# Optimization experiments

Measured on AMD Instinct MI355X. Metric: run time of the kernel, lower is better.

Reference implementation:

```python
import jax, jax.numpy as jnp
import numpy as np
from jax import lax

PRE_NMS = 2000
POST_NMS = 300
NMS_THRESH = 0.7
MIN_SIZE = 16.0
SCALE = 1.0
RATIOS = (0.5, 1.0, 2.0)
SCALES = (8, 16, 32)
STRIDES = (8, 16, 32)
FEAT_HW = ((100, 100), (50, 50), (25, 25))
BASE_SIZE = 16.0


def _anchor_base(scale):
    py = px = BASE_SIZE / 2.0
    ab = np.zeros((len(RATIOS), 4), dtype=np.float32)
    for i, r in enumerate(RATIOS):
        h = BASE_SIZE * scale * np.sqrt(r)
        w = BASE_SIZE * scale * np.sqrt(1.0 / r)
        ab[i] = [py - h / 2.0, px - w / 2.0, py + h / 2.0, px + w / 2.0]
    return ab


def _enum_anchors():
    out = []
    for lvl in range(3):
        ab = _anchor_base(SCALES[lvl])
        hh, ww = FEAT_HW[lvl]
        fs = STRIDES[lvl]
        sy = np.arange(0, hh * fs, fs)
        sx = np.arange(0, ww * fs, fs)
        sx, sy = np.meshgrid(sx, sy)
        shift = np.stack((sy.ravel(), sx.ravel(), sy.ravel(), sx.ravel()), axis=1)
        a = ab[None, :, :] + shift[:, None, :]  # [K, A, 4]
        out.append(a.reshape(-1, 4).astype(np.float32))
    return np.concatenate(out, axis=0)  # [39375, 4]


def setup_inputs() -> dict:
    key = jax.random.key(0)
    ks = jax.random.split(key, 8)
    inp = {
        "feat0": jax.random.normal(ks[0], (2, 256, 100, 100), jnp.float32),
        "feat1": jax.random.normal(ks[1], (2, 256, 50, 50), jnp.float32),
        "feat2": jax.random.normal(ks[2], (2, 256, 25, 25), jnp.float32),
        "conv_w": 0.01 * jax.random.normal(ks[3], (256, 256, 3, 3), jnp.float32),
        "conv_b": jnp.zeros((256,), jnp.float32),
        "score_w": 0.01 * jax.random.normal(ks[4], (6, 256), jnp.float32),
        "score_b": jnp.zeros((6,), jnp.float32),
        "loc_w": 0.01 * jax.random.normal(ks[5], (12, 256), jnp.float32),
        "loc_b": jnp.zeros((12,), jnp.float32),
        "anchors": jnp.asarray(_enum_anchors()),
        "img_h": 800,
        "img_w": 800,
    }
    return inp


def loc2bbox(anchors, loc):
    src_h = anchors[:, 2] - anchors[:, 0]
    src_w = anchors[:, 3] - anchors[:, 1]
    ctr_y = anchors[:, 0] + 0.5 * src_h
    ctr_x = anchors[:, 1] + 0.5 * src_w
    dy, dx, dh, dw = loc[:, 0], loc[:, 1], loc[:, 2], loc[:, 3]
    cy = dy * src_h + ctr_y
    cx = dx * src_w + ctr_x
    h = jnp.exp(dh) * src_h
    w = jnp.exp(dw) * src_w
    return jnp.stack([cy - 0.5 * h, cx - 0.5 * w, cy + 0.5 * h, cx + 0.5 * w], axis=1)


def _iou_matrix(boxes):
    area = (boxes[:, 2] - boxes[:, 0]) * (boxes[:, 3] - boxes[:, 1])
    tl = jnp.maximum(boxes[:, None, :2], boxes[None, :, :2])
    br = jnp.minimum(boxes[:, None, 2:], boxes[None, :, 2:])
    wh = jnp.clip(br - tl, 0.0)
    inter = wh[..., 0] * wh[..., 1]
    return inter / (area[:, None] + area[None, :] - inter + 1e-12)


def _nms_keep(boxes, valid):
    # greedy NMS over score-sorted boxes; returns boolean keep mask
    M = _iou_matrix(boxes)  # [PRE_NMS, PRE_NMS]
    idx = jnp.arange(PRE_NMS)

    def body(i, suppressed):
        sup_later = (~suppressed[i]) & (M[i] > NMS_THRESH) & (idx > i)
        return suppressed | sup_later

    suppressed = lax.fori_loop(0, PRE_NMS, body, ~valid)
    return ~suppressed


def _propose(loc, fg, anchors, img_h, img_w):
    roi = loc2bbox(anchors, loc)  # [S, 4]
    roi = jnp.stack([
        jnp.clip(roi[:, 0], 0.0, float(img_h)),
        jnp.clip(roi[:, 1], 0.0, float(img_w)),
        jnp.clip(roi[:, 2], 0.0, float(img_h)),
        jnp.clip(roi[:, 3], 0.0, float(img_w)),
    ], axis=1)
    hs = roi[:, 2] - roi[:, 0]
    ws = roi[:, 3] - roi[:, 1]
    valid = (hs >= MIN_SIZE * SCALE) & (ws >= MIN_SIZE * SCALE)
    sc = jnp.where(valid, fg, -jnp.inf)
    top_sc, top_idx = lax.top_k(sc, PRE_NMS)
    boxes = roi[top_idx]
    keep = _nms_keep(boxes, jnp.isfinite(top_sc))
    # stable move of kept boxes to the front (indices are unique)
    order = jnp.argsort(jnp.where(keep, jnp.arange(PRE_NMS), PRE_NMS))[:POST_NMS]
    rois = boxes[order] * keep[order][:, None].astype(boxes.dtype)  # zero-pad invalid
    return rois  # [POST_NMS, 4]


def reference(feat0, feat1, feat2, conv_w, conv_b, score_w, score_b, loc_w, loc_b, anchors, img_h, img_w):
    feats = [feat0, feat1, feat2]
    n = feat0.shape[0]
    locs, scores, fgs = [], [], []
    dn = ("NCHW", "OIHW", "NCHW")
    for x in feats:
        h = jax.nn.relu(
            lax.conv_general_dilated(x, conv_w, (1, 1), "SAME", dimension_numbers=dn)
            + conv_b[None, :, None, None]
        )
        hh, ww = h.shape[2], h.shape[3]
        loc = jnp.einsum("nchw,oc->nhwo", h, loc_w) + loc_b  # [n,h,w,12]
        sc = jnp.einsum("nchw,oc->nhwo", h, score_w) + score_b  # [n,h,w,6]
        fg = jax.nn.softmax(sc.reshape(n, hh, ww, 3, 2), axis=-1)[..., 1]
        locs.append(loc.reshape(n, -1, 4))
        scores.append(sc.reshape(n, -1, 2))
        fgs.append(fg.reshape(n, -1))
    rpn_locs = jnp.concatenate(locs, axis=1)      # [n, S, 4]
    rpn_scores = jnp.concatenate(scores, axis=1)  # [n, S, 2]
    rpn_fg = jnp.concatenate(fgs, axis=1)         # [n, S]
    rois = jax.vmap(lambda l, f: _propose(l, f, anchors, img_h, img_w))(rpn_locs, rpn_fg)
    rois = rois.reshape(-1, 4)  # [n*POST_NMS, 4]
    roi_indices = jnp.repeat(jnp.arange(n, dtype=jnp.int32), POST_NMS)
    return rpn_locs, rpn_scores, rois, roi_indices, anchors
```

## Files before the change

kernel.cpp:

```cpp
#include <hip/hip_runtime.h>
#include <hip/hip_fp16.h>
#include <cstdint>
#include <cstddef>

typedef unsigned long long u64;
typedef unsigned int u32;
typedef __attribute__((ext_vector_type(8))) _Float16 f16x8;
typedef __attribute__((ext_vector_type(4))) float f32x4;

#define NANCHORS 39375
#define PRE_NMS  2000
#define POST_NMS 300
#define CAND_CAP 4096
#define MPAD 2048
#define UNEG 0x007FFFFFu
#define NPIX 26250

__device__ __forceinline__ u32 f2u(float f) {
  u32 u = __float_as_uint(f);
  return (u & 0x80000000u) ? ~u : (u | 0x80000000u);
}

#define GLOAD16(gp, lp) __builtin_amdgcn_global_load_lds( \
    (const __attribute__((address_space(1))) u32*)(const void*)(gp), \
    (__attribute__((address_space(3))) u32*)(void*)(lp), 16, 0, 0)

#define DPP_SUM16(v) do { \
  v += __int_as_float(__builtin_amdgcn_update_dpp(0, __float_as_int(v), 0x128, 0xf, 0xf, true)); \
  v += __int_as_float(__builtin_amdgcn_update_dpp(0, __float_as_int(v), 0x124, 0xf, 0xf, true)); \
  v += __int_as_float(__builtin_amdgcn_update_dpp(0, __float_as_int(v), 0x122, 0xf, 0xf, true)); \
  v += __int_as_float(__builtin_amdgcn_update_dpp(0, __float_as_int(v), 0x121, 0xf, 0xf, true)); \
} while (0)

__global__ __launch_bounds__(64) void ringzero_kernel(short* __restrict__ xh, short* __restrict__ xl) {
  int t = blockIdx.x;
  int b = t / 712, i = t % 712;
  int W2, AB, ABS;
  if (i < 404)      { W2 = 102; AB = 0;       ABS = 2663424; }
  else if (i < 608) { i -= 404; W2 = 52; AB = 5326848; ABS = 692224; }
  else              { i -= 608; W2 = 27; AB = 6711296; ABS = 186624; }
  int y, x;
  if (i < W2)          { y = 0;      x = i; }
  else if (i < 2 * W2) { y = W2 - 1; x = i - W2; }
  else { int j = i - 2 * W2; y = 1 + (j >> 1); x = (j & 1) ? (W2 - 1) : 0; }
  size_t base = (size_t)AB + (size_t)b * ABS + ((size_t)(y * W2 + x)) * 256 + threadIdx.x * 4;
  int2 z = {0, 0};
  *(int2*)(xh + base) = z;
  *(int2*)(xl + base) = z;
}

__global__ __launch_bounds__(256) void xsplit_kernel(
    const float* __restrict__ f0, const float* __restrict__ f1, const float* __restrict__ f2,
    short* __restrict__ xh, short* __restrict__ xl)
{
  __shared__ float tile[64][65];
  int t = blockIdx.x;
  int HW, W, W2, np; const float* fp; int AB, ABS;
  if (t < 1256)      { HW = 10000; W = 100; W2 = 102; np = 157; fp = f0; AB = 0;       ABS = 2663424; }
  else if (t < 1576) { t -= 1256; HW = 2500; W = 50; W2 = 52; np = 40; fp = f1; AB = 5326848; ABS = 692224; }
  else               { t -= 1576; HW = 625;  W = 25; W2 = 27; np = 10; fp = f2; AB = 6711296; ABS = 186624; }
  int posb = t % np, r = t / np;
  int ci0 = (r & 3) * 64, b = r >> 2;
  int pos0 = posb * 64;
  int tid = threadIdx.x, lane = tid & 63, w = tid >> 6;
  int rp = pos0 + lane; if (rp >= HW) rp = HW - 1;
  const float* src = fp + (size_t)(b * 256 + ci0) * HW;
#pragma unroll
  for (int p = 0; p < 16; ++p) {
    int cl = w * 16 + p;
    tile[cl][lane] = src[(size_t)cl * HW + rp];
  }
  __syncthreads();
  int pix = tid >> 2, cq = tid & 3;
  int pos = pos0 + pix;
  if (pos < HW) {
    int y = pos / W, x = pos - y * W;
    size_t ob = (size_t)AB + (size_t)b * ABS + ((size_t)((y + 1) * W2 + (x + 1))) * 256 + ci0 + cq * 16;
    __align__(16) short hs[16], ls[16];
#pragma unroll
    for (int j = 0; j < 16; ++j) {
      float v = tile[cq * 16 + j][pix];
      __half h = __float2half(v);
      __half l = __float2half((v - __half2float(h)) * 2048.0f);
      hs[j] = __half_as_short(h);
      ls[j] = __half_as_short(l);
    }
    *(int4*)(xh + ob) = ((int4*)hs)[0];
    *(int4*)(xh + ob + 8) = ((int4*)hs)[1];
    *(int4*)(xl + ob) = ((int4*)ls)[0];
    *(int4*)(xl + ob + 8) = ((int4*)ls)[1];
  }
}

__global__ __launch_bounds__(256) void wsplit_kernel(
    const float* __restrict__ w, short* __restrict__ wh, short* __restrict__ wl)
{
  int idx = blockIdx.x * 256 + threadIdx.x;
  int tap = idx >> 16, co = (idx >> 8) & 255, ci = idx & 255;
  float v = w[(size_t)co * 2304 + ci * 9 + tap];
  __half h = __float2half(v);
  __half l = __float2half((v - __half2float(h)) * 2048.0f);
  wh[idx] = __half_as_short(h);
  wl[idx] = __half_as_short(l);
}

__global__ __launch_bounds__(256, 2) void gemmconv_kernel(
    const short* __restrict__ xh, const short* __restrict__ xl,
    const short* __restrict__ wh, const short* __restrict__ wl,
    const float* __restrict__ bias,
    const float* __restrict__ loc_w, const float* __restrict__ score_w,
    float* __restrict__ proj2)
{
  __shared__ __align__(16) short smem[32768];

  int lb = (blockIdx.x & 7) * 52 + (blockIdx.x >> 3);
  int HW, W, W2, AB, ABS, lvlbase;
  if (lb < 316)      { HW = 10000; W = 100; W2 = 102; AB = 0;       ABS = 2663424; lvlbase = 0; }
  else if (lb < 396) { lb -= 316; HW = 2500; W = 50; W2 = 52; AB = 5326848; ABS = 692224; lvlbase = 10000; }
  else               { lb -= 396; HW = 625;  W = 25; W2 = 27; AB = 6711296; ABS = 186624; lvlbase = 12500; }
  int mb = lb >> 2, b = (lb >> 1) & 1, nb = lb & 1;
  int pos0 = mb * 128, co0 = nb * 128;

  int tid = threadIdx.x;
  int s = tid & 7, mrow = tid >> 3;
  int aoff[4], boff[4];
#pragma unroll
  for (int i = 0; i < 4; ++i) {
    int m = i * 32 + mrow;
    int pos = pos0 + m; if (pos >= HW) pos = HW - 1;
    int y = pos / W, x = pos - y * W;
    aoff[i] = AB + b * ABS + (y * W2 + x) * 256 + ((s ^ (m & 7)) << 3);
    boff[i] = ((co0 + m) << 8) + ((s ^ (m & 7)) << 3);
  }
  int wv = tid >> 6, lane = tid & 63;
  int lr = lane & 15, lk = lane >> 4;
  int wr = wv >> 1, wc = wv & 1;
  int rA0 = wr * 64 + lr, rB0 = wc * 64 + lr;
  int cs = (lr & 7) << 4;
  int c0 = ((lk * 16) ^ cs) >> 1;
  int c1 = ((64 + lk * 16) ^ cs) >> 1;

  f32x4 acc1[4][4], acc2[4][4];
  f32x4 zro = {0.f, 0.f, 0.f, 0.f};
#pragma unroll
  for (int i = 0; i < 4; ++i)
#pragma unroll
    for (int j = 0; j < 4; ++j) { acc1[i][j] = zro; acc2[i][j] = zro; }

  for (int cc = 0; cc < 36; ++cc) {
    int tap = cc >> 2, cq = cc & 3;
    int ty = tap / 3, tx = tap - ty * 3;
    int adel = (ty * W2 + tx) * 256 + (cq << 6);
    int bdel = (tap << 16) + (cq << 6);
    if (cc) __syncthreads();
#pragma unroll
    for (int i = 0; i < 4; ++i) {
      int d = i * 2048 + wv * 512;
      GLOAD16(xh + aoff[i] + adel, smem + d);
      GLOAD16(xl + aoff[i] + adel, smem + 8192 + d);
      GLOAD16(wh + boff[i] + bdel, smem + 16384 + d);
      GLOAD16(wl + boff[i] + bdel, smem + 24576 + d);
    }
    __syncthreads();
#pragma unroll
    for (int k2 = 0; k2 < 2; ++k2) {
      int ck = k2 ? c1 : c0;
      f16x8 ah[4], al[4], bh[4], bl[4];
#pragma unroll
      for (int q = 0; q < 4; ++q) {
        int ro = (rA0 + q * 16) * 64 + ck;
        ah[q] = *(const f16x8*)(smem + ro);
        al[q] = *(const f16x8*)(smem + 8192 + ro);
        int rb = (rB0 + q * 16) * 64 + ck;
        bh[q] = *(const f16x8*)(smem + 16384 + rb);
        bl[q] = *(const f16x8*)(smem + 24576 + rb);
      }
#pragma unroll
      for (int m4 = 0; m4 < 4; ++m4)
#pragma unroll
        for (int n4 = 0; n4 < 4; ++n4) {
          acc1[m4][n4] = __builtin_amdgcn_mfma_f32_16x16x32_f16(ah[m4], bh[n4], acc1[m4][n4], 0, 0, 0);
          acc2[m4][n4] = __builtin_amdgcn_mfma_f32_16x16x32_f16(ah[m4], bl[n4], acc2[m4][n4], 0, 0, 0);
          acc2[m4][n4] = __builtin_amdgcn_mfma_f32_16x16x32_f16(al[m4], bh[n4], acc2[m4][n4], 0, 0, 0);
        }
    }
  }

  float br[4];
#pragma unroll
  for (int n4 = 0; n4 < 4; ++n4) br[n4] = bias[co0 + wc * 64 + n4 * 16 + lr];
  float* pslot = proj2 + (size_t)(nb * 2 + wc) * NPIX * 20;
  int Pbase = b * 13125 + lvlbase;

#pragma unroll 1
  for (int half = 0; half < 2; ++half) {
    float wpr[4][9];
#pragma unroll
    for (int n4 = 0; n4 < 4; ++n4) {
      int c = co0 + wc * 64 + n4 * 16 + lr;
#pragma unroll
      for (int oo = 0; oo < 9; ++oo) {
        int o = half * 9 + oo;
        wpr[n4][oo] = (o < 12) ? loc_w[o * 256 + c] : score_w[(o - 12) * 256 + c];
      }
    }
#pragma unroll
    for (int m4 = 0; m4 < 4; ++m4) {
#pragma unroll
      for (int j = 0; j < 4; ++j) {
        int pos = pos0 + wr * 64 + m4 * 16 + lk * 4 + j;
        bool ok = pos < HW;
        float po[9];
#pragma unroll
        for (int oo = 0; oo < 9; ++oo) po[oo] = 0.f;
#pragma unroll
        for (int n4 = 0; n4 < 4; ++n4) {
          float h = acc1[m4][n4][j] + acc2[m4][n4][j] * 4.8828125e-4f + br[n4];
          h = ok ? fmaxf(h, 0.f) : 0.f;
#pragma unroll
          for (int oo = 0; oo < 9; ++oo) po[oo] = fmaf(h, wpr[n4][oo], po[oo]);
        }
#pragma unroll
        for (int oo = 0; oo < 9; ++oo) DPP_SUM16(po[oo]);
        if (ok && lr < 9) {
          float out = po[0];
#pragma unroll
          for (int oo = 1; oo < 9; ++oo) if (lr == oo) out = po[oo];
          pslot[(size_t)(Pbase + pos) * 20 + half * 9 + lr] = out;
        }
      }
    }
  }
}

__global__ __launch_bounds__(256) void decode_kernel(
    const float* __restrict__ proj2, const float* __restrict__ loc_b, const float* __restrict__ score_b,
    const float* __restrict__ anchors, const int* __restrict__ imgh, const int* __restrict__ imgw,
    float* __restrict__ out_locs, float* __restrict__ out_scores,
    float* __restrict__ boxes, u32* __restrict__ ukey)
{
  int P = blockIdx.x * 256 + threadIdx.x;
  if (P >= NPIX) return;
  int b = P / 13125, r = P % 13125;
  int pos, base_row;
  if (r < 10000)      { pos = r;         base_row = 0; }
  else if (r < 12500) { pos = r - 10000; base_row = 30000; }
  else                { pos = r - 12500; base_row = 37500; }

  float sarr[18];
#pragma unroll
  for (int o = 0; o < 18; ++o)
    sarr[o] = proj2[(size_t)P * 20 + o] + proj2[(size_t)NPIX * 20 + (size_t)P * 20 + o]
            + proj2[(size_t)2 * NPIX * 20 + (size_t)P * 20 + o]
            + proj2[(size_t)3 * NPIX * 20 + (size_t)P * 20 + o];

  float IH = (float)(*imgh), IW = (float)(*imgw);
#pragma unroll
  for (int a = 0; a < 3; ++a) {
    float l0 = sarr[4 * a + 0] + loc_b[4 * a + 0];
    float l1 = sarr[4 * a + 1] + loc_b[4 * a + 1];
    float l2 = sarr[4 * a + 2] + loc_b[4 * a + 2];
    float l3 = sarr[4 * a + 3] + loc_b[4 * a + 3];
    float sc0 = sarr[12 + 2 * a + 0] + score_b[2 * a + 0];
    float sc1 = sarr[12 + 2 * a + 1] + score_b[2 * a + 1];

    int row = base_row + pos * 3 + a;
    size_t g = (size_t)b * NANCHORS + row;
    *(float4*)(out_locs + g * 4) = make_float4(l0, l1, l2, l3);
    out_scores[g * 2 + 0] = sc0; out_scores[g * 2 + 1] = sc1;

    float mx = fmaxf(sc0, sc1);
    float e0 = expf(sc0 - mx), e1 = expf(sc1 - mx);
    float fg = e1 / (e0 + e1);

    const float* an = anchors + (size_t)row * 4;
    float a0 = an[0], a1 = an[1], a2 = an[2], a3 = an[3];
    float sh = a2 - a0, sw = a3 - a1;
    float cy = a0 + 0.5f * sh, cx = a1 + 0.5f * sw;
    float ncy = l0 * sh + cy, ncx = l1 * sw + cx;
    float nh = expf(l2) * sh, nw = expf(l3) * sw;
    float y1 = fminf(fmaxf(ncy - 0.5f * nh, 0.f), IH);
    float x1 = fminf(fmaxf(ncx - 0.5f * nw, 0.f), IW);
    float y2 = fminf(fmaxf(ncy + 0.5f * nh, 0.f), IH);
    float x2 = fminf(fmaxf(ncx + 0.5f * nw, 0.f), IW);
    bool valid = ((y2 - y1) >= 16.0f) && ((x2 - x1) >= 16.0f);
    float scm = valid ? fg : -__builtin_inff();

    *(float4*)(boxes + g * 4) = make_float4(y1, x1, y2, x2);
    ukey[g] = f2u(scm);
  }
}

__global__ void copyf_kernel(const float* __restrict__ a, float* __restrict__ o, int n) {
  int t = blockIdx.x * 256 + threadIdx.x;
  if (t < n) o[t] = a[t];
}

__global__ __launch_bounds__(1024) void selectsort_kernel(
    const u32* __restrict__ ukey, const float* __restrict__ boxes,
    float* __restrict__ topbox, u64* __restrict__ sup0)
{
  int b = blockIdx.x, tid = threadIdx.x;
  int lane = tid & 63;
  const u32* u = ukey + (size_t)b * NANCHORS;
  __shared__ u32 hist[256];
  __shared__ u32 sh_prefix;
  __shared__ int sh_rem;
  __shared__ int sh_cnt;
  __shared__ u64 key[CAND_CAP];
  __shared__ unsigned char validf[2048];

  u32 val[39];
#pragma unroll
  for (int k = 0; k < 38; ++k) val[k] = u[tid + k * 1024];
  val[38] = (tid < 463) ? u[tid + 38912] : 0u;

  u32 prefix = 0; int rem = PRE_NMS;
#pragma unroll 1
  for (int pass = 0; pass < 4; ++pass) {
    int shift = 24 - 8 * pass;
    if (tid < 256) hist[tid] = 0;
    __syncthreads();
    u32 himask = (pass == 0) ? 0u : (0xFFFFFFFFu << (shift + 8));
    u32 pmask = prefix & himask;
#pragma unroll
    for (int k = 0; k < 39; ++k) {
      bool live = (k < 38) || (tid < 463);
      u32 v = val[k];
      bool m = live && ((v & himask) == pmask);
      u32 bin = (v >> shift) & 255u;
      u64 actm = __ballot(m);
      if (actm) {
        int src = __ffsll(actm) - 1;
        u32 binf = __shfl(bin, src, 64);
        bool same = m && (bin == binf);
        u64 sm = __ballot(same);
        if (same) {
          if (lane == __ffsll(sm) - 1)
            atomicAdd(&hist[binf], (u32)__popcll(sm));
        } else if (m) {
          atomicAdd(&hist[bin], 1u);
        }
      }
    }
    __syncthreads();
    if (tid < 64) {
      u32 h0 = hist[4 * lane], h1 = hist[4 * lane + 1];
      u32 h2 = hist[4 * lane + 2], h3 = hist[4 * lane + 3];
      u32 L = h0 + h1 + h2 + h3;
      u32 SS = L;
#pragma unroll
      for (int off = 1; off < 64; off <<= 1) {
        u32 tv = __shfl_down(SS, off, 64);
        if (lane + off < 64) SS += tv;
      }
      u32 T = SS - L;
      u32 s3 = h3 + T, s2 = h2 + s3, s1 = h1 + s2, s0 = h0 + s1;
      u32 sv[5] = {s0, s1, s2, s3, T};
#pragma unroll
      for (int j = 0; j < 4; ++j) {
        if ((int)sv[j] >= rem && (int)sv[j + 1] < rem) {
          sh_prefix = prefix | ((u32)(4 * lane + j) << shift);
          sh_rem = rem - (int)sv[j + 1];
        }
      }
    }
    __syncthreads();
    prefix = sh_prefix; rem = sh_rem;
  }

  if (tid == 0) sh_cnt = 0;
  __syncthreads();
#pragma unroll
  for (int k = 0; k < 39; ++k) {
    bool live = (k < 38) || (tid < 463);
    u32 v = val[k];
    bool c = live && (v >= prefix);
    u64 mask = __ballot(c);
    if (mask) {
      int leader = __ffsll(mask) - 1;
      int cntw = __popcll(mask);
      int base = 0;
      if (lane == leader) base = atomicAdd(&sh_cnt, cntw);
      base = __shfl(base, leader, 64);
      int p = base + (int)__popcll(mask & ((1ull << lane) - 1ull));
      if (c && p < CAND_CAP)
        key[p] = ((u64)v << 32) | (u32)(~(u32)(tid + k * 1024));
    }
  }
  __syncthreads();
  int cnt = (sh_cnt < CAND_CAP) ? sh_cnt : CAND_CAP;
  for (int t = tid; t < CAND_CAP; t += 1024)
    if (t >= cnt) key[t] = 0ull;
  __syncthreads();

  u32 n = (cnt <= 2048) ? 2048u : (u32)CAND_CAP;
  for (u32 k = 2; k <= n; k <<= 1) {
    for (u32 j = k >> 1; j > 0; j >>= 1) {
      __syncthreads();
      for (u32 t = tid; t < n; t += 1024) {
        u32 ixj = t ^ j;
        if (ixj > t) {
          u64 a = key[t], c = key[ixj];
          bool desc = ((t & k) == 0);
          if (desc ? (a < c) : (a > c)) { key[t] = c; key[ixj] = a; }
        }
      }
    }
  }
  __syncthreads();

  for (int t = tid; t < 2048; t += 1024) {
    unsigned char vf = 0;
    if (t < PRE_NMS) {
      u64 kk = key[t];
      u32 uu = (u32)(kk >> 32);
      float* tb = topbox + ((size_t)b * PRE_NMS + t) * 4;
      if (uu != 0u) {
        u32 idx = ~((u32)kk);
        const float* bp = boxes + ((size_t)b * NANCHORS + idx) * 4;
        tb[0] = bp[0]; tb[1] = bp[1]; tb[2] = bp[2]; tb[3] = bp[3];
        vf = (uu != UNEG) ? 1 : 0;
      } else {
        tb[0] = 0.f; tb[1] = 0.f; tb[2] = 0.f; tb[3] = 0.f;
      }
    }
    validf[t] = vf;
  }
  __syncthreads();
  if (tid < 32) {
    u64 m = 0;
    for (int bit = 0; bit < 64; ++bit) {
      int j = tid * 64 + bit;
      if (j >= PRE_NMS || !validf[j]) m |= (1ull << bit);
    }
    sup0[b * 32 + tid] = m;
  }
}

__global__ __launch_bounds__(256) void iou_kernel(const float* __restrict__ topbox, u32* __restrict__ M32)
{
  int t = blockIdx.x * 256 + threadIdx.x;
  int b = blockIdx.y;
  int w = t / 2000, i = t % 2000;
  const float* tb = topbox + (size_t)b * PRE_NMS * 4;
  const float* bi = tb + (size_t)i * 4;
  float iy1 = bi[0], ix1 = bi[1], iy2 = bi[2], ix2 = bi[3];
  float ai = (iy2 - iy1) * (ix2 - ix1);
  u64 m = 0;
  for (int bit = 0; bit < 64; ++bit) {
    int j = w * 64 + bit;
    if (j < PRE_NMS && j > i) {
      const float* bj = tb + (size_t)j * 4;
      float ty = fmaxf(iy1, bj[0]), tx = fmaxf(ix1, bj[1]);
      float by = fminf(iy2, bj[2]), bx = fminf(ix2, bj[3]);
      float hh = fmaxf(by - ty, 0.f), ww = fmaxf(bx - tx, 0.f);
      float inter = hh * ww;
      float aj = (bj[2] - bj[0]) * (bj[3] - bj[1]);
      float iou = inter / (ai + aj - inter + 1e-12f);
      if (iou > 0.7f) m |= (1ull << bit);
    }
  }
  u32* out = M32 + (size_t)b * MPAD * 64;
  out[(size_t)(2 * w)     * MPAD + i] = (u32)m;
  out[(size_t)(2 * w + 1) * MPAD + i] = (u32)(m >> 32);
}

__global__ __launch_bounds__(320) void final_kernel(
    const u32* __restrict__ M32, const u64* __restrict__ sup0, const float* __restrict__ topbox,
    float* __restrict__ rois, float* __restrict__ roiidx)
{
  int b = blockIdx.x, tid = threadIdx.x;
  __shared__ u32 supl[64];
  __shared__ int ord[POST_NMS];
  __shared__ int cnt_s;

  if (tid < 64) {
    int l = tid;
    const u32* col = M32 + (size_t)b * MPAD * 64 + (size_t)l * MPAD;
    u32 sup = ((const u32*)sup0)[b * 64 + l];
    uint4 A[16], B[16];
#pragma unroll
    for (int k = 0; k < 16; ++k) A[k] = *(const uint4*)(col + 4 * k);

#define NMS_PROC(buf, cc) do {                                                     \
  _Pragma("unroll")                                                                \
  for (int rr = 0; rr < 64; ++rr) {                                                \
    u32 d = ((rr & 3) == 0) ? buf[rr >> 2].x : ((rr & 3) == 1) ? buf[rr >> 2].y :  \
            ((rr & 3) == 2) ? buf[rr >> 2].z : buf[rr >> 2].w;                     \
    u32 sb = (u32)__builtin_amdgcn_readlane((int)sup, 2 * (cc) + (rr >> 5));       \
    u32 m = ((sb >> (rr & 31)) & 1u) - 1u;                                         \
    sup |= m & d;                                                                  \
  } } while (0)

    for (int c = 0; c < 32; c += 2) {
#pragma unroll
      for (int k = 0; k < 16; ++k) B[k] = *(const uint4*)(col + (c + 1) * 64 + 4 * k);
      NMS_PROC(A, c);
      if (c + 2 < 32) {
#pragma unroll
        for (int k = 0; k < 16; ++k) A[k] = *(const uint4*)(col + (c + 2) * 64 + 4 * k);
      }
      NMS_PROC(B, c + 1);
    }
    supl[l] = sup;
  }
  __syncthreads();
  if (tid == 0) {
    int cnt = 0;
    for (int w = 0; w < 64 && cnt < POST_NMS; ++w) {
      u32 kept = ~supl[w];
      while (kept && cnt < POST_NMS) {
        int bit = __builtin_ctz(kept); kept &= kept - 1;
        ord[cnt++] = w * 32 + bit;
      }
    }
    cnt_s = cnt;
  }
  __syncthreads();
  if (tid < POST_NMS) {
    float v0 = 0.f, v1 = 0.f, v2 = 0.f, v3 = 0.f;
    if (tid < cnt_s) {
      const float* tb = topbox + ((size_t)b * PRE_NMS + ord[tid]) * 4;
      v0 = tb[0]; v1 = tb[1]; v2 = tb[2]; v3 = tb[3];
    }
    float* r = rois + ((size_t)b * POST_NMS + tid) * 4;
    r[0] = v0; r[1] = v1; r[2] = v2; r[3] = v3;
    roiidx[b * POST_NMS + tid] = (float)b;
  }
}

extern "C" void kernel_launch(void* const* d_in, const int* in_sizes, int n_in,
                              void* d_out, int out_size, void* d_ws, size_t ws_size,
                              hipStream_t stream) {
  const float* feat0   = (const float*)d_in[0];
  const float* feat1   = (const float*)d_in[1];
  const float* feat2   = (const float*)d_in[2];
  const float* conv_w  = (const float*)d_in[3];
  const float* conv_b  = (const float*)d_in[4];
  const float* score_w = (const float*)d_in[5];
  const float* score_b = (const float*)d_in[6];
  const float* loc_w   = (const float*)d_in[7];
  const float* loc_b   = (const float*)d_in[8];
  const float* anchors = (const float*)d_in[9];
  const int*   img_h   = (const int*)d_in[10];
  const int*   img_w   = (const int*)d_in[11];

  float* out_f       = (float*)d_out;
  float* out_locs    = out_f;
  float* out_scores  = out_f + 315000;
  float* out_rois    = out_f + 472500;
  float* out_roiidx  = out_f + 474900;
  float* out_anchors = out_f + 475500;

  char* p = (char*)d_ws;
  short* xth = (short*)p;     p += (size_t)7084544 * 2;
  short* xtl = (short*)p;     p += (size_t)7084544 * 2;
  short* wsh = (short*)p;     p += (size_t)589824 * 2;
  short* wsl = (short*)p;     p += (size_t)589824 * 2;
  float* proj2 = (float*)p;   p += (size_t)4 * NPIX * 20 * 4;
  float* boxes = (float*)p;   p += (size_t)315000 * 4;
  u32* ukey = (u32*)p;        p += (size_t)78752 * 4;
  float* topbox = (float*)p;  p += (size_t)16000 * 4;
  u32* M32 = (u32*)p;         p += (size_t)2 * MPAD * 64 * 4;
  u64* sup0 = (u64*)p;        p += 64 * 8;

  ringzero_kernel<<<1424, 64, 0, stream>>>(xth, xtl);
  xsplit_kernel<<<1656, 256, 0, stream>>>(feat0, feat1, feat2, xth, xtl);
  wsplit_kernel<<<2304, 256, 0, stream>>>(conv_w, wsh, wsl);
  gemmconv_kernel<<<416, 256, 0, stream>>>(xth, xtl, wsh, wsl, conv_b, loc_w, score_w, proj2);
  decode_kernel<<<(NPIX + 255) / 256, 256, 0, stream>>>(
      proj2, loc_b, score_b, anchors, img_h, img_w,
      out_locs, out_scores, boxes, ukey);
  copyf_kernel<<<(157500 + 255) / 256, 256, 0, stream>>>(anchors, out_anchors, 157500);
  selectsort_kernel<<<2, 1024, 0, stream>>>(ukey, boxes, topbox, sup0);
  iou_kernel<<<dim3(250, 2), 256, 0, stream>>>(topbox, M32);
  final_kernel<<<2, 320, 0, stream>>>(M32, sup0, topbox, out_rois, out_roiidx);
}
```

Baseline: 362.9 us.

## Merge prep kernels into one launch and fuse decode into gemmconv via tickets

```diff
diff --git a/kernel.cpp b/kernel.cpp
--- a/kernel.cpp
+++ b/kernel.cpp
@@ -32,76 +32,83 @@
   v += __int_as_float(__builtin_amdgcn_update_dpp(0, __float_as_int(v), 0x121, 0xf, 0xf, true)); \
 } while (0)
 
-__global__ __launch_bounds__(64) void ringzero_kernel(short* __restrict__ xh, short* __restrict__ xl) {
-  int t = blockIdx.x;
-  int b = t / 712, i = t % 712;
-  int W2, AB, ABS;
-  if (i < 404)      { W2 = 102; AB = 0;       ABS = 2663424; }
-  else if (i < 608) { i -= 404; W2 = 52; AB = 5326848; ABS = 692224; }
-  else              { i -= 608; W2 = 27; AB = 6711296; ABS = 186624; }
-  int y, x;
-  if (i < W2)          { y = 0;      x = i; }
-  else if (i < 2 * W2) { y = W2 - 1; x = i - W2; }
-  else { int j = i - 2 * W2; y = 1 + (j >> 1); x = (j & 1) ? (W2 - 1) : 0; }
-  size_t base = (size_t)AB + (size_t)b * ABS + ((size_t)(y * W2 + x)) * 256 + threadIdx.x * 4;
-  int2 z = {0, 0};
-  *(int2*)(xh + base) = z;
-  *(int2*)(xl + base) = z;
-}
-
-__global__ __launch_bounds__(256) void xsplit_kernel(
+__global__ __launch_bounds__(256) void prep_kernel(
     const float* __restrict__ f0, const float* __restrict__ f1, const float* __restrict__ f2,
-    short* __restrict__ xh, short* __restrict__ xl)
+    const float* __restrict__ w, const float* __restrict__ anchors,
+    short* __restrict__ xh, short* __restrict__ xl,
+    short* __restrict__ wh, short* __restrict__ wl,
+    float* __restrict__ out_anchors, int* __restrict__ ticket)
 {
-  __shared__ float tile[64][65];
-  int t = blockIdx.x;
-  int HW, W, W2, np; const float* fp; int AB, ABS;
-  if (t < 1256)      { HW = 10000; W = 100; W2 = 102; np = 157; fp = f0; AB = 0;       ABS = 2663424; }
-  else if (t < 1576) { t -= 1256; HW = 2500; W = 50; W2 = 52; np = 40; fp = f1; AB = 5326848; ABS = 692224; }
-  else               { t -= 1576; HW = 625;  W = 25; W2 = 27; np = 10; fp = f2; AB = 6711296; ABS = 186624; }
-  int posb = t % np, r = t / np;
-  int ci0 = (r & 3) * 64, b = r >> 2;
-  int pos0 = posb * 64;
-  int tid = threadIdx.x, lane = tid & 63, w = tid >> 6;
-  int rp = pos0 + lane; if (rp >= HW) rp = HW - 1;
-  const float* src = fp + (size_t)(b * 256 + ci0) * HW;
-#pragma unroll
-  for (int p = 0; p < 16; ++p) {
-    int cl = w * 16 + p;
-    tile[cl][lane] = src[(size_t)cl * HW + rp];
-  }
-  __syncthreads();
-  int pix = tid >> 2, cq = tid & 3;
-  int pos = pos0 + pix;
-  if (pos < HW) {
-    int y = pos / W, x = pos - y * W;
-    size_t ob = (size_t)AB + (size_t)b * ABS + ((size_t)((y + 1) * W2 + (x + 1))) * 256 + ci0 + cq * 16;
-    __align__(16) short hs[16], ls[16];
-#pragma unroll
-    for (int j = 0; j < 16; ++j) {
-      float v = tile[cq * 16 + j][pix];
-      __half h = __float2half(v);
-      __half l = __float2half((v - __half2float(h)) * 2048.0f);
-      hs[j] = __half_as_short(h);
-      ls[j] = __half_as_short(l);
-    }
-    *(int4*)(xh + ob) = ((int4*)hs)[0];
-    *(int4*)(xh + ob + 8) = ((int4*)hs)[1];
-    *(int4*)(xl + ob) = ((int4*)ls)[0];
-    *(int4*)(xl + ob + 8) = ((int4*)ls)[1];
-  }
-}
-
-__global__ __launch_bounds__(256) void wsplit_kernel(
-    const float* __restrict__ w, short* __restrict__ wh, short* __restrict__ wl)
-{
-  int idx = blockIdx.x * 256 + threadIdx.x;
-  int tap = idx >> 16, co = (idx >> 8) & 255, ci = idx & 255;
-  float v = w[(size_t)co * 2304 + ci * 9 + tap];
-  __half h = __float2half(v);
-  __half l = __float2half((v - __half2float(h)) * 2048.0f);
-  wh[idx] = __half_as_short(h);
-  wl[idx] = __half_as_short(l);
+  int blk = blockIdx.x;
+  int tid = threadIdx.x;
+  if (blk < 1656) {
+    __shared__ float tile[64][65];
+    int t = blk;
+    int HW, W, W2, np; const float* fp; int AB, ABS;
+    if (t < 1256)      { HW = 10000; W = 100; W2 = 102; np = 157; fp = f0; AB = 0;       ABS = 2663424; }
+    else if (t < 1576) { t -= 1256; HW = 2500; W = 50; W2 = 52; np = 40; fp = f1; AB = 5326848; ABS = 692224; }
+    else               { t -= 1576; HW = 625;  W = 25; W2 = 27; np = 10; fp = f2; AB = 6711296; ABS = 186624; }
+    int posb = t % np, r = t / np;
+    int ci0 = (r & 3) * 64, b = r >> 2;
+    int pos0 = posb * 64;
+    int lane = tid & 63, wv = tid >> 6;
+    int rp = pos0 + lane; if (rp >= HW) rp = HW - 1;
+    const float* src = fp + (size_t)(b * 256 + ci0) * HW;
+#pragma unroll
+    for (int p = 0; p < 16; ++p) {
+      int cl = wv * 16 + p;
+      tile[cl][lane] = src[(size_t)cl * HW + rp];
+    }
+    __syncthreads();
+    int pix = tid >> 2, cq = tid & 3;
+    int pos = pos0 + pix;
+    if (pos < HW) {
+      int y = pos / W, x = pos - y * W;
+      size_t ob = (size_t)AB + (size_t)b * ABS + ((size_t)((y + 1) * W2 + (x + 1))) * 256 + ci0 + cq * 16;
+      __align__(16) short hs[16], ls[16];
+#pragma unroll
+      for (int j = 0; j < 16; ++j) {
+        float v = tile[cq * 16 + j][pix];
+        __half h = __float2half(v);
+        __half l = __float2half((v - __half2float(h)) * 2048.0f);
+        hs[j] = __half_as_short(h);
+        ls[j] = __half_as_short(l);
+      }
+      *(int4*)(xh + ob) = ((int4*)hs)[0];
+      *(int4*)(xh + ob + 8) = ((int4*)hs)[1];
+      *(int4*)(xl + ob) = ((int4*)ls)[0];
+      *(int4*)(xl + ob + 8) = ((int4*)ls)[1];
+    }
+  } else if (blk < 3960) {
+    int idx = (blk - 1656) * 256 + tid;
+    int tap = idx >> 16, co = (idx >> 8) & 255, ci = idx & 255;
+    float v = w[(size_t)co * 2304 + ci * 9 + tap];
+    __half h = __float2half(v);
+    __half l = __float2half((v - __half2float(h)) * 2048.0f);
+    wh[idx] = __half_as_short(h);
+    wl[idx] = __half_as_short(l);
+  } else if (blk < 4316) {
+    int g = (blk - 3960) * 256 + tid;
+    int t = g >> 6, ln = g & 63;
+    int b = t / 712, i = t % 712;
+    int W2, AB, ABS;
+    if (i < 404)      { W2 = 102; AB = 0;       ABS = 2663424; }
+    else if (i < 608) { i -= 404; W2 = 52; AB = 5326848; ABS = 692224; }
+    else              { i -= 608; W2 = 27; AB = 6711296; ABS = 186624; }
+    int y, x;
+    if (i < W2)          { y = 0;      x = i; }
+    else if (i < 2 * W2) { y = W2 - 1; x = i - W2; }
+    else { int j = i - 2 * W2; y = 1 + (j >> 1); x = (j & 1) ? (W2 - 1) : 0; }
+    size_t base = (size_t)AB + (size_t)b * ABS + ((size_t)(y * W2 + x)) * 256 + ln * 4;
+    int2 z = {0, 0};
+    *(int2*)(xh + base) = z;
+    *(int2*)(xl + base) = z;
+  } else if (blk < 4932) {
+    int t = (blk - 4316) * 256 + tid;
+    if (t < 157500) out_anchors[t] = anchors[t];
+  } else {
+    if (tid < 256) ticket[tid] = 0;
+  }
 }
 
 __global__ __launch_bounds__(256, 2) void gemmconv_kernel(
@@ -109,15 +116,20 @@
     const short* __restrict__ wh, const short* __restrict__ wl,
     const float* __restrict__ bias,
     const float* __restrict__ loc_w, const float* __restrict__ score_w,
-    float* __restrict__ proj2)
+    const float* __restrict__ loc_b, const float* __restrict__ score_b,
+    const float* __restrict__ anchors, const int* __restrict__ imgh, const int* __restrict__ imgw,
+    float* __restrict__ proj2, int* __restrict__ ticket,
+    float* __restrict__ out_locs, float* __restrict__ out_scores,
+    float* __restrict__ boxes, u32* __restrict__ ukey)
 {
   __shared__ __align__(16) short smem[32768];
 
   int lb = (blockIdx.x & 7) * 52 + (blockIdx.x >> 3);
-  int HW, W, W2, AB, ABS, lvlbase;
-  if (lb < 316)      { HW = 10000; W = 100; W2 = 102; AB = 0;       ABS = 2663424; lvlbase = 0; }
-  else if (lb < 396) { lb -= 316; HW = 2500; W = 50; W2 = 52; AB = 5326848; ABS = 692224; lvlbase = 10000; }
-  else               { lb -= 396; HW = 625;  W = 25; W2 = 27; AB = 6711296; ABS = 186624; lvlbase = 12500; }
+  int tix = lb >> 1;
+  int HW, W, W2, AB, ABS, lvlbase, base_row;
+  if (lb < 316)      { HW = 10000; W = 100; W2 = 102; AB = 0;       ABS = 2663424; lvlbase = 0;     base_row = 0; }
+  else if (lb < 396) { lb -= 316; HW = 2500; W = 50; W2 = 52; AB = 5326848; ABS = 692224; lvlbase = 10000; base_row = 30000; }
+  else               { lb -= 396; HW = 625;  W = 25; W2 = 27; AB = 6711296; ABS = 186624; lvlbase = 12500; base_row = 37500; }
   int mb = lb >> 2, b = (lb >> 1) & 1, nb = lb & 1;
   int pos0 = mb * 128, co0 = nb * 128;
 
@@ -231,69 +243,63 @@
       }
     }
   }
-}
-
-__global__ __launch_bounds__(256) void decode_kernel(
-    const float* __restrict__ proj2, const float* __restrict__ loc_b, const float* __restrict__ score_b,
-    const float* __restrict__ anchors, const int* __restrict__ imgh, const int* __restrict__ imgw,
-    float* __restrict__ out_locs, float* __restrict__ out_scores,
-    float* __restrict__ boxes, u32* __restrict__ ukey)
-{
-  int P = blockIdx.x * 256 + threadIdx.x;
-  if (P >= NPIX) return;
-  int b = P / 13125, r = P % 13125;
-  int pos, base_row;
-  if (r < 10000)      { pos = r;         base_row = 0; }
-  else if (r < 12500) { pos = r - 10000; base_row = 30000; }
-  else                { pos = r - 12500; base_row = 37500; }
-
-  float sarr[18];
-#pragma unroll
-  for (int o = 0; o < 18; ++o)
-    sarr[o] = proj2[(size_t)P * 20 + o] + proj2[(size_t)NPIX * 20 + (size_t)P * 20 + o]
-            + proj2[(size_t)2 * NPIX * 20 + (size_t)P * 20 + o]
-            + proj2[(size_t)3 * NPIX * 20 + (size_t)P * 20 + o];
-
-  float IH = (float)(*imgh), IW = (float)(*imgw);
-#pragma unroll
-  for (int a = 0; a < 3; ++a) {
-    float l0 = sarr[4 * a + 0] + loc_b[4 * a + 0];
-    float l1 = sarr[4 * a + 1] + loc_b[4 * a + 1];
-    float l2 = sarr[4 * a + 2] + loc_b[4 * a + 2];
-    float l3 = sarr[4 * a + 3] + loc_b[4 * a + 3];
-    float sc0 = sarr[12 + 2 * a + 0] + score_b[2 * a + 0];
-    float sc1 = sarr[12 + 2 * a + 1] + score_b[2 * a + 1];
-
-    int row = base_row + pos * 3 + a;
-    size_t g = (size_t)b * NANCHORS + row;
-    *(float4*)(out_locs + g * 4) = make_float4(l0, l1, l2, l3);
-    out_scores[g * 2 + 0] = sc0; out_scores[g * 2 + 1] = sc1;
-
-    float mx = fmaxf(sc0, sc1);
-    float e0 = expf(sc0 - mx), e1 = expf(sc1 - mx);
-    float fg = e1 / (e0 + e1);
-
-    const float* an = anchors + (size_t)row * 4;
-    float a0 = an[0], a1 = an[1], a2 = an[2], a3 = an[3];
-    float sh = a2 - a0, sw = a3 - a1;
-    float cy = a0 + 0.5f * sh, cx = a1 + 0.5f * sw;
-    float ncy = l0 * sh + cy, ncx = l1 * sw + cx;
-    float nh = expf(l2) * sh, nw = expf(l3) * sw;
-    float y1 = fminf(fmaxf(ncy - 0.5f * nh, 0.f), IH);
-    float x1 = fminf(fmaxf(ncx - 0.5f * nw, 0.f), IW);
-    float y2 = fminf(fmaxf(ncy + 0.5f * nh, 0.f), IH);
-    float x2 = fminf(fmaxf(ncx + 0.5f * nw, 0.f), IW);
-    bool valid = ((y2 - y1) >= 16.0f) && ((x2 - x1) >= 16.0f);
-    float scm = valid ? fg : -__builtin_inff();
-
-    *(float4*)(boxes + g * 4) = make_float4(y1, x1, y2, x2);
-    ukey[g] = f2u(scm);
-  }
-}
-
-__global__ void copyf_kernel(const float* __restrict__ a, float* __restrict__ o, int n) {
-  int t = blockIdx.x * 256 + threadIdx.x;
-  if (t < n) o[t] = a[t];
+
+  __shared__ int sh_do;
+  __threadfence();
+  if (tid == 0) sh_do = (atomicAdd(&ticket[tix], 1) == 1) ? 1 : 0;
+  __syncthreads();
+  if (sh_do) {
+    __threadfence();
+    int px = tid;
+    if (px < 128) {
+      int pos = pos0 + px;
+      if (pos < HW) {
+        int P = b * 13125 + lvlbase + pos;
+        float sarr[18];
+#pragma unroll
+        for (int o = 0; o < 18; ++o)
+          sarr[o] = proj2[(size_t)P * 20 + o]
+                  + proj2[(size_t)NPIX * 20 + (size_t)P * 20 + o]
+                  + proj2[(size_t)2 * NPIX * 20 + (size_t)P * 20 + o]
+                  + proj2[(size_t)3 * NPIX * 20 + (size_t)P * 20 + o];
+        float IH = (float)(*imgh), IW = (float)(*imgw);
+#pragma unroll
+        for (int a = 0; a < 3; ++a) {
+          float l0 = sarr[4 * a + 0] + loc_b[4 * a + 0];
+          float l1 = sarr[4 * a + 1] + loc_b[4 * a + 1];
+          float l2 = sarr[4 * a + 2] + loc_b[4 * a + 2];
+          float l3 = sarr[4 * a + 3] + loc_b[4 * a + 3];
+          float sc0 = sarr[12 + 2 * a + 0] + score_b[2 * a + 0];
+          float sc1 = sarr[12 + 2 * a + 1] + score_b[2 * a + 1];
+
+          int row = base_row + pos * 3 + a;
+          size_t g = (size_t)b * NANCHORS + row;
+          *(float4*)(out_locs + g * 4) = make_float4(l0, l1, l2, l3);
+          out_scores[g * 2 + 0] = sc0; out_scores[g * 2 + 1] = sc1;
+
+          float mx = fmaxf(sc0, sc1);
+          float e0 = expf(sc0 - mx), e1 = expf(sc1 - mx);
+          float fg = e1 / (e0 + e1);
+
+          const float* an = anchors + (size_t)row * 4;
+          float a0 = an[0], a1 = an[1], a2 = an[2], a3 = an[3];
+          float sh = a2 - a0, sw = a3 - a1;
+          float cy = a0 + 0.5f * sh, cx = a1 + 0.5f * sw;
+          float ncy = l0 * sh + cy, ncx = l1 * sw + cx;
+          float nh = expf(l2) * sh, nw = expf(l3) * sw;
+          float y1 = fminf(fmaxf(ncy - 0.5f * nh, 0.f), IH);
+          float x1 = fminf(fmaxf(ncx - 0.5f * nw, 0.f), IW);
+          float y2 = fminf(fmaxf(ncy + 0.5f * nh, 0.f), IH);
+          float x2 = fminf(fmaxf(ncx + 0.5f * nw, 0.f), IW);
+          bool valid = ((y2 - y1) >= 16.0f) && ((x2 - x1) >= 16.0f);
+          float scm = valid ? fg : -__builtin_inff();
+
+          *(float4*)(boxes + g * 4) = make_float4(y1, x1, y2, x2);
+          ukey[g] = f2u(scm);
+        }
+      }
+    }
+  }
 }
 
 __global__ __launch_bounds__(1024) void selectsort_kernel(
@@ -564,15 +570,14 @@
   float* topbox = (float*)p;  p += (size_t)16000 * 4;
   u32* M32 = (u32*)p;         p += (size_t)2 * MPAD * 64 * 4;
   u64* sup0 = (u64*)p;        p += 64 * 8;
-
-  ringzero_kernel<<<1424, 64, 0, stream>>>(xth, xtl);
-  xsplit_kernel<<<1656, 256, 0, stream>>>(feat0, feat1, feat2, xth, xtl);
-  wsplit_kernel<<<2304, 256, 0, stream>>>(conv_w, wsh, wsl);
-  gemmconv_kernel<<<416, 256, 0, stream>>>(xth, xtl, wsh, wsl, conv_b, loc_w, score_w, proj2);
-  decode_kernel<<<(NPIX + 255) / 256, 256, 0, stream>>>(
-      proj2, loc_b, score_b, anchors, img_h, img_w,
+  int* ticket = (int*)p;      p += 256 * 4;
+
+  prep_kernel<<<4933, 256, 0, stream>>>(
+      feat0, feat1, feat2, conv_w, anchors, xth, xtl, wsh, wsl, out_anchors, ticket);
+  gemmconv_kernel<<<416, 256, 0, stream>>>(
+      xth, xtl, wsh, wsl, conv_b, loc_w, score_w, loc_b, score_b,
+      anchors, img_h, img_w, proj2, ticket,
       out_locs, out_scores, boxes, ukey);
-  copyf_kernel<<<(157500 + 255) / 256, 256, 0, stream>>>(anchors, out_anchors, 157500);
   selectsort_kernel<<<2, 1024, 0, stream>>>(ukey, boxes, topbox, sup0);
   iou_kernel<<<dim3(250, 2), 256, 0, stream>>>(topbox, M32);
   final_kernel<<<2, 320, 0, stream>>>(M32, sup0, topbox, out_rois, out_roiidx);
```

After: 408.0 us. 1.12x slower.
